# Kernel tuning notes

Measured on AMD Instinct MI355X. Metric: run time of the kernel, lower is better.

The kernel has to match this reference:

```python
import jax, jax.numpy as jnp
import numpy as np
import math

D_MODEL = 1024
NUM_HEADS = 16
D_K = D_MODEL // NUM_HEADS
THETA = 10000.0
B, T = 2, 2048


def _trunc_normal(key, shape, std):
    # truncated normal in [-3std, 3std]
    return jax.random.truncated_normal(key, -3.0, 3.0, shape, jnp.float32) * std


def setup_inputs() -> dict:
    key = jax.random.key(0)
    ks = jax.random.split(key, 6)
    sigma = math.sqrt(2.0 / (D_MODEL + D_MODEL))
    x = jax.random.normal(ks[0], (B, T, D_MODEL), jnp.float32)
    Wq = _trunc_normal(ks[1], (D_MODEL, D_MODEL), sigma)  # [out, in]
    Wk = _trunc_normal(ks[2], (D_MODEL, D_MODEL), sigma)
    Wv = _trunc_normal(ks[3], (D_MODEL, D_MODEL), sigma)
    Wo = _trunc_normal(ks[4], (D_MODEL, D_MODEL), sigma)
    token_positions = jnp.arange(T, dtype=jnp.int64 if jax.config.read('jax_enable_x64') else jnp.int32)
    return {"x": x, "Wq": Wq, "Wk": Wk, "Wv": Wv, "Wo": Wo,
            "token_positions": token_positions}


def _rotate_half(x):
    x0 = x[..., ::2]
    x1 = x[..., 1::2]
    return jnp.stack((-x1, x0), axis=-1).reshape(x.shape)


def _rope(x, token_positions):
    # x: [B, H, T, d_k]; token_positions: [T]
    inv_freq = 1.0 / (THETA ** (jnp.arange(0, D_K, 2, dtype=jnp.float32) / D_K))
    ang = token_positions.astype(jnp.float32)[:, None] * inv_freq  # [T, d_k/2]
    cos = jnp.repeat(jnp.cos(ang), 2, axis=-1)  # [T, d_k]
    sin = jnp.repeat(jnp.sin(ang), 2, axis=-1)
    xdtype = x.dtype
    xf = x.astype(jnp.float32)
    return (xf * cos + _rotate_half(xf) * sin).astype(xdtype)


def reference(x, Wq, Wk, Wv, Wo, token_positions):
    b, t, _ = x.shape

    def proj_split(W):
        h = jnp.einsum('btd,od->bto', x, W)
        return h.reshape(b, t, NUM_HEADS, D_K).transpose(0, 2, 1, 3)  # [B,H,T,d_k]

    Q = _rope(proj_split(Wq), token_positions)
    K = _rope(proj_split(Wk), token_positions)
    V = proj_split(Wv)

    scores = jnp.einsum('bhqd,bhkd->bhqk', Q, K) / math.sqrt(D_K)
    causal = jnp.tril(jnp.ones((t, t), dtype=bool))  # [T,T]
    scores = jnp.where(causal, scores, -jnp.inf)
    weights = jax.nn.softmax(scores, axis=-1)
    attn = jnp.einsum('bhqk,bhkd->bhqd', weights, V)  # [B,H,T,d_v]
    merged = attn.transpose(0, 2, 1, 3).reshape(b, t, D_MODEL)
    return jnp.einsum('btd,od->bto', merged, Wo)
```

## Files before the change

### kernel.cpp

```cpp
#include <hip/hip_runtime.h>
#include <hip/hip_fp16.h>
#include <cstdint>
#include <cstddef>

#define DMODEL 1024
#define NHEADS 16
#define DKH    64
#define SEQT   2048
#define NBATCH 2
#define MTOT   (NBATCH*SEQT)

#define QSCALE 0.1803368801111204f

using h16   = _Float16;
using h16x2 = __attribute__((ext_vector_type(2))) h16;
using h16x4 = __attribute__((ext_vector_type(4))) h16;
using h16x8 = __attribute__((ext_vector_type(8))) h16;
using f32x4 = __attribute__((ext_vector_type(4))) float;
using fp16x2_native = __attribute__((ext_vector_type(2))) __fp16;

using as1_void = __attribute__((address_space(1))) void;
using as3_void = __attribute__((address_space(3))) void;

__device__ __forceinline__ void gll16(void* lds, const void* g) {
  __builtin_amdgcn_global_load_lds((const as1_void*)g, (as3_void*)lds, 16, 0, 0);
}

__device__ __forceinline__ h16x2 pkrtz(float a, float b) {
  fp16x2_native t = __builtin_amdgcn_cvt_pkrtz(a, b);
  h16x2 r; r[0] = (h16)t[0]; r[1] = (h16)t[1]; return r;
}

__device__ __forceinline__ h16 hx2exp(h16 x) {
  __half r = hexp2(*(__half*)&x);
  return *(h16*)&r;
}

__device__ __forceinline__ h16x4 cvt4(const float4 v) {
  h16x4 o; o[0] = (h16)v.x; o[1] = (h16)v.y; o[2] = (h16)v.z; o[3] = (h16)v.w; return o;
}

__global__ void prep_kernel(const float4* __restrict__ x,
                            const float4* __restrict__ Wq, const float4* __restrict__ Wk,
                            const float4* __restrict__ Wv, const float4* __restrict__ Wo,
                            h16x4* __restrict__ xb,
                            h16x4* __restrict__ wqb, h16x4* __restrict__ wkb,
                            h16x4* __restrict__ wvb, h16x4* __restrict__ wob,
                            float* __restrict__ ctab, float* __restrict__ stab) {
  const int tid  = blockIdx.x * blockDim.x + threadIdx.x;
  const int nthr = gridDim.x * blockDim.x;
  const int NX4 = MTOT * DMODEL / 4;
  const int NW4 = DMODEL * DMODEL / 4;
  for (int i = tid; i < NX4; i += nthr) xb[i] = cvt4(x[i]);
  for (int i = tid; i < NW4; i += nthr) {
    wqb[i] = cvt4(Wq[i]);
    wkb[i] = cvt4(Wk[i]);
    wvb[i] = cvt4(Wv[i]);
    wob[i] = cvt4(Wo[i]);
  }
  for (int i = tid; i < SEQT * 32; i += nthr) {
    const int t = i >> 5, fi = i & 31;
    float inv = __expf(-0.28782313662425575f * (float)fi);
    float ang = (float)t * inv;
    float s, c;
    sincosf(ang, &s, &c);
    ctab[i] = c; stab[i] = s;
  }
}

__device__ __forceinline__ void gemm128_bt(const h16* __restrict__ A, const h16* __restrict__ Bt,
                                           int m0, int n0, h16* Al, h16* Bl, f32x4 acc[4][4]) {
  const int tid  = threadIdx.x;
  const int lane = tid & 63;
  const int wv   = tid >> 6;
  const int wm = (wv >> 1) * 64, wn = (wv & 1) * 64;
  const int lr = lane & 15, lk = (lane >> 4) * 8;
  const int srow = tid >> 2, scol = (tid & 3) * 8;
  const h16* a0 = A  + (size_t)(m0 + srow) * DMODEL + scol;
  const h16* a1 = a0 + (size_t)64 * DMODEL;
  const h16* b0 = Bt + (size_t)(n0 + srow) * DMODEL + scol;
  const h16* b1 = b0 + (size_t)64 * DMODEL;
  h16* alds0 = Al + wv * 512;
  h16* alds1 = Al + 2048 + wv * 512;
  h16* blds0 = Bl + wv * 512;
  h16* blds1 = Bl + 2048 + wv * 512;

  for (int k0 = 0; k0 < DMODEL; k0 += 32) {
    __syncthreads();
    gll16(alds0, a0 + k0);
    gll16(alds1, a1 + k0);
    gll16(blds0, b0 + k0);
    gll16(blds1, b1 + k0);
    __syncthreads();
    h16x8 af[4], bfr[4];
#pragma unroll
    for (int i = 0; i < 4; ++i) {
      af[i]  = *(const h16x8*)(Al + (wm + i * 16 + lr) * 32 + lk);
      bfr[i] = *(const h16x8*)(Bl + (wn + i * 16 + lr) * 32 + lk);
    }
#pragma unroll
    for (int i = 0; i < 4; ++i)
#pragma unroll
      for (int j = 0; j < 4; ++j)
        acc[i][j] = __builtin_amdgcn_mfma_f32_16x16x32_f16(af[i], bfr[j], acc[i][j], 0, 0, 0);
  }
}

__global__ __launch_bounds__(256, 2) void qkv_kernel(
    const h16* __restrict__ xb,
    const h16* __restrict__ wqb, const h16* __restrict__ wkb, const h16* __restrict__ wvb,
    const float* __restrict__ ctab, const float* __restrict__ stab,
    h16* __restrict__ Qb, h16* __restrict__ Kb, h16* __restrict__ Vt) {
  __shared__ h16 Al[128 * 32], Bl[128 * 32];
  const int which = blockIdx.z;
  const h16* W = (which == 0) ? wqb : (which == 1) ? wkb : wvb;
  const int m0 = blockIdx.x * 128, n0 = blockIdx.y * 128;
  f32x4 acc[4][4];
  const f32x4 zero4 = {0.f, 0.f, 0.f, 0.f};
#pragma unroll
  for (int i = 0; i < 4; ++i)
#pragma unroll
    for (int j = 0; j < 4; ++j) acc[i][j] = zero4;

  gemm128_bt(xb, W, m0, n0, Al, Bl, acc);

  const int lane = threadIdx.x & 63, wv = threadIdx.x >> 6;
  const int wm = (wv >> 1) * 64, wn = (wv & 1) * 64;
  const int lr4 = ((lane >> 4) << 2), lc = lane & 15;
  if (which == 2) {
#pragma unroll
    for (int i = 0; i < 4; ++i) {
      const int m = m0 + wm + i * 16 + lr4;
      const int b = m >> 11, t = m & (SEQT - 1);
#pragma unroll
      for (int j = 0; j < 4; ++j) {
        const int n = n0 + wn + j * 16 + lc;
        const int h = n >> 6, d = n & 63;
        h16x4 o4;
#pragma unroll
        for (int r = 0; r < 4; ++r) o4[r] = (h16)acc[i][j][r];
        *(h16x4*)&Vt[((size_t)(b * NHEADS + h) * DKH + d) * SEQT + t] = o4;
      }
    }
  } else {
#pragma unroll
    for (int i = 0; i < 4; ++i) {
#pragma unroll
      for (int j = 0; j < 4; ++j) {
        const int n = n0 + wn + j * 16 + lc;
        const int h = n >> 6, d = n & 63;
#pragma unroll
        for (int r = 0; r < 4; ++r) {
          const int m = m0 + wm + i * 16 + lr4 + r;
          const int b = m >> 11, t = m & (SEQT - 1);
          float v = acc[i][j][r];
          float pv = __shfl_xor(v, 1);
          const int fi = d >> 1;
          float c = ctab[t * 32 + fi], s = stab[t * 32 + fi];
          float res = (d & 1) ? (v * c + pv * s) : (v * c - pv * s);
          if (which == 0) res *= QSCALE;
          h16* dst = (which == 0) ? Qb : Kb;
          dst[((size_t)(b * NHEADS + h) * SEQT + t) * DKH + d] = (h16)res;
        }
      }
    }
  }
}

__global__ __launch_bounds__(256, 4) void attn_kernel(
    const h16* __restrict__ Qb, const h16* __restrict__ Kb,
    const h16* __restrict__ Vt, h16* __restrict__ Mg) {
  __shared__ h16 Kl[128][76];
  __shared__ h16 Vl[64][140];
  const int linear = blockIdx.x + 32 * blockIdx.y;
  const int v   = linear & 7;
  const int p   = linear >> 3;
  const int w   = p >> 5;
  const int c32 = p & 31;
  const int u   = (c32 + w) & 3;
  const int bh  = c32;
  const int qt  = (u == 0) ? v : (u == 1) ? (15 - v) : (u == 2) ? (16 + v) : (31 - v);
  const int b = bh >> 4, h = bh & 15;
  const int tid = threadIdx.x, lane = tid & 63, wv = tid >> 6;
  const int lr = lane & 15, lg = lane >> 4;
  const int q0 = qt * 64;
  const int qbase = q0 + wv * 16;
  const int q = qbase + lr;
  const h16* Qp = Qb + ((size_t)bh * SEQT + qbase) * DKH;
  const h16* Kp = Kb + (size_t)bh * SEQT * DKH;
  const h16* Vp = Vt + (size_t)bh * DKH * SEQT;

  h16x8 qf[2];
#pragma unroll
  for (int kk = 0; kk < 2; ++kk)
    qf[kk] = *(const h16x8*)(Qp + lr * DKH + kk * 32 + lg * 8);

  float mrow = -3.0e38f, lsum = 0.f;
  f32x4 o[4];
  const f32x4 zero4 = {0.f, 0.f, 0.f, 0.f};
#pragma unroll
  for (int di = 0; di < 4; ++di) o[di] = zero4;

  const int sr = tid >> 2, sc = (tid & 3) * 16;
  uint4 ka0, ka1, ka2, ka3;
  uint4 va0, va1, va2, va3;

#define KISSUE(k0_) {                                                      \
    const h16* kb_ = Kp + (size_t)(k0_) * DKH;                             \
    ka0 = *(const uint4*)(kb_ + (size_t)sr * DKH + sc);                    \
    ka1 = *(const uint4*)(kb_ + (size_t)sr * DKH + sc + 8);                \
    ka2 = *(const uint4*)(kb_ + (size_t)(64 + sr) * DKH + sc);             \
    ka3 = *(const uint4*)(kb_ + (size_t)(64 + sr) * DKH + sc + 8);         \
  }
#define KWRITE() {                                                         \
    *(uint4*)&Kl[sr][sc]          = ka0;                                   \
    *(uint4*)&Kl[sr][sc + 8]      = ka1;                                   \
    *(uint4*)&Kl[64 + sr][sc]     = ka2;                                   \
    *(uint4*)&Kl[64 + sr][sc + 8] = ka3;                                   \
  }
#define VISSUE(k0_) {                                                      \
    const h16* vb_ = Vp + (k0_);                                           \
    va0 = *(const uint4*)(vb_ + (size_t)sr * SEQT + sc);                   \
    va1 = *(const uint4*)(vb_ + (size_t)sr * SEQT + sc + 8);               \
    va2 = *(const uint4*)(vb_ + (size_t)sr * SEQT + 64 + sc);              \
    va3 = *(const uint4*)(vb_ + (size_t)sr * SEQT + 64 + sc + 8);          \
  }
#define VWRITE() {                                                         \
    *(uint4*)&Vl[sr][sc]          = va0;                                   \
    *(uint4*)&Vl[sr][sc + 8]      = va1;                                   \
    *(uint4*)&Vl[sr][64 + sc]     = va2;                                   \
    *(uint4*)&Vl[sr][64 + sc + 8] = va3;                                   \
  }

  KISSUE(0); VISSUE(0);
  KWRITE(); VWRITE();
  __syncthreads();

  const int nkt = (qt >> 1) + 1;
  for (int kt = 0; kt < nkt; ++kt) {
    const int k0 = kt * 128;
    const bool more = (kt + 1 < nkt);

    if (more) { KISSUE(k0 + 128); __builtin_amdgcn_sched_barrier(0); }

    f32x4 s[8];
    __builtin_amdgcn_s_setprio(1);
#pragma unroll
    for (int ni = 0; ni < 8; ++ni) {
      s[ni] = zero4;
#pragma unroll
      for (int kk = 0; kk < 2; ++kk) {
        h16x8 kf = *(const h16x8*)&Kl[ni * 16 + lr][kk * 32 + lg * 8];
        s[ni] = __builtin_amdgcn_mfma_f32_16x16x32_f16(kf, qf[kk], s[ni], 0, 0, 0);
      }
    }
    __builtin_amdgcn_s_setprio(0);

    __syncthreads();
    if (more) {
      KWRITE();
      VISSUE(k0 + 128); __builtin_amdgcn_sched_barrier(0);
    }

    if (kt == nkt - 1) {
#pragma unroll
      for (int ni = 0; ni < 8; ++ni)
#pragma unroll
        for (int r = 0; r < 4; ++r) {
          const int key = k0 + ni * 16 + lg * 4 + r;
          if (key > q) s[ni][r] = -3.0e38f;
        }
    }

    h16x4 s16[8];
#pragma unroll
    for (int ni = 0; ni < 8; ++ni) {
      h16x2 lo = pkrtz(s[ni][0], s[ni][1]);
      h16x2 hi = pkrtz(s[ni][2], s[ni][3]);
      s16[ni][0] = lo[0]; s16[ni][1] = lo[1]; s16[ni][2] = hi[0]; s16[ni][3] = hi[1];
    }

    h16x4 t0 = __builtin_elementwise_max(s16[0], s16[1]);
    h16x4 t1 = __builtin_elementwise_max(s16[2], s16[3]);
    h16x4 t2 = __builtin_elementwise_max(s16[4], s16[5]);
    h16x4 t3 = __builtin_elementwise_max(s16[6], s16[7]);
    h16x4 t4 = __builtin_elementwise_max(__builtin_elementwise_max(t0, t1),
                                         __builtin_elementwise_max(t2, t3));
    h16 mh = t4[0] > t4[1] ? t4[0] : t4[1];
    h16 m2 = t4[2] > t4[3] ? t4[2] : t4[3];
    mh = mh > m2 ? mh : m2;
    float mx = (float)mh;
    mx = fmaxf(mx, __shfl_xor(mx, 16));
    mx = fmaxf(mx, __shfl_xor(mx, 32));
    if (mx > mrow + 9.0f) {
      const float scl = exp2f(mrow - mx);
      mrow = mx;
      lsum *= scl;
#pragma unroll
      for (int di = 0; di < 4; ++di)
#pragma unroll
        for (int r = 0; r < 4; ++r) o[di][r] *= scl;
    }

    const h16 m16 = (h16)mrow;
    h16x4 mv; mv[0] = m16; mv[1] = m16; mv[2] = m16; mv[3] = m16;
    h16x4 pb[8];
#pragma unroll
    for (int ni = 0; ni < 8; ++ni) {
      h16x4 d = s16[ni] - mv;
      pb[ni][0] = hx2exp(d[0]); pb[ni][1] = hx2exp(d[1]);
      pb[ni][2] = hx2exp(d[2]); pb[ni][3] = hx2exp(d[3]);
    }

    {
      h16x4 a0 = pb[0] + pb[1];
      h16x4 a1 = pb[2] + pb[3];
      h16x4 a2 = pb[4] + pb[5];
      h16x4 a3 = pb[6] + pb[7];
      h16x4 a4 = (a0 + a1) + (a2 + a3);
      float rs = (float)a4[0] + (float)a4[1] + (float)a4[2] + (float)a4[3];
      rs += __shfl_xor(rs, 16);
      rs += __shfl_xor(rs, 32);
      lsum += rs;
    }

    __builtin_amdgcn_s_setprio(1);
#pragma unroll
    for (int ni = 0; ni < 8; ++ni) {
#pragma unroll
      for (int di = 0; di < 4; ++di) {
        h16x4 va = *(const h16x4*)&Vl[di * 16 + lr][ni * 16 + lg * 4];
        o[di] = __builtin_amdgcn_mfma_f32_16x16x16f16(va, pb[ni], o[di], 0, 0, 0);
      }
    }
    __builtin_amdgcn_s_setprio(0);

    __syncthreads();
    if (more) VWRITE();
  }
#undef KISSUE
#undef KWRITE
#undef VISSUE
#undef VWRITE

  __syncthreads();
  const float inv = 1.0f / lsum;
#pragma unroll
  for (int di = 0; di < 4; ++di) {
    h16x2 lo = pkrtz(o[di][0] * inv, o[di][1] * inv);
    h16x2 hi = pkrtz(o[di][2] * inv, o[di][3] * inv);
    h16x4 o4; o4[0] = lo[0]; o4[1] = lo[1]; o4[2] = hi[0]; o4[3] = hi[1];
    *(h16x4*)&Kl[wv * 16 + lr][di * 16 + lg * 4] = o4;
  }
  __syncthreads();
  {
    const int row = tid >> 2, c0 = (tid & 3) * 16;
    h16* dst = Mg + ((size_t)(b * SEQT + q0 + row)) * DMODEL + h * DKH + c0;
    *(uint4*)dst       = *(const uint4*)&Kl[row][c0];
    *(uint4*)(dst + 8) = *(const uint4*)&Kl[row][c0 + 8];
  }
}

__global__ __launch_bounds__(256, 2) void proj_kernel(
    const h16* __restrict__ Mg, const h16* __restrict__ wob, float* __restrict__ out) {
  __shared__ h16 Al[128 * 32], Bl[128 * 32];
  const int m0 = blockIdx.x * 128, n0 = blockIdx.y * 128;
  f32x4 acc[4][4];
  const f32x4 zero4 = {0.f, 0.f, 0.f, 0.f};
#pragma unroll
  for (int i = 0; i < 4; ++i)
#pragma unroll
    for (int j = 0; j < 4; ++j) acc[i][j] = zero4;

  gemm128_bt(Mg, wob, m0, n0, Al, Bl, acc);

  const int lane = threadIdx.x & 63, wv = threadIdx.x >> 6;
  const int wm = (wv >> 1) * 64, wn = (wv & 1) * 64;
  const int lr4 = ((lane >> 4) << 2), lc = lane & 15;
#pragma unroll
  for (int i = 0; i < 4; ++i)
#pragma unroll
    for (int j = 0; j < 4; ++j) {
      const int n = n0 + wn + j * 16 + lc;
#pragma unroll
      for (int r = 0; r < 4; ++r) {
        const int m = m0 + wm + i * 16 + lr4 + r;
        out[(size_t)m * DMODEL + n] = acc[i][j][r];
      }
    }
}

extern "C" void kernel_launch(void* const* d_in, const int* in_sizes, int n_in,
                              void* d_out, int out_size, void* d_ws, size_t ws_size,
                              hipStream_t stream) {
  (void)in_sizes; (void)n_in; (void)out_size; (void)ws_size;
  const float* x  = (const float*)d_in[0];
  const float* Wq = (const float*)d_in[1];
  const float* Wk = (const float*)d_in[2];
  const float* Wv = (const float*)d_in[3];
  const float* Wo = (const float*)d_in[4];
  float* out = (float*)d_out;

  char* w = (char*)d_ws;
  h16* xb  = (h16*)w; w += (size_t)MTOT * DMODEL * 2;
  h16* wqb = (h16*)w; w += (size_t)DMODEL * DMODEL * 2;
  h16* wkb = (h16*)w; w += (size_t)DMODEL * DMODEL * 2;
  h16* wvb = (h16*)w; w += (size_t)DMODEL * DMODEL * 2;
  h16* wob = (h16*)w; w += (size_t)DMODEL * DMODEL * 2;
  h16* Qb  = (h16*)w; w += (size_t)MTOT * DMODEL * 2;
  h16* Kb  = (h16*)w; w += (size_t)MTOT * DMODEL * 2;
  h16* Vt  = (h16*)w; w += (size_t)MTOT * DMODEL * 2;
  h16* Mg  = (h16*)w; w += (size_t)MTOT * DMODEL * 2;
  float* ctab = (float*)w; w += (size_t)SEQT * 32 * 4;
  float* stab = (float*)w; w += (size_t)SEQT * 32 * 4;

  prep_kernel<<<1024, 256, 0, stream>>>((const float4*)x, (const float4*)Wq, (const float4*)Wk,
                                        (const float4*)Wv, (const float4*)Wo,
                                        (h16x4*)xb, (h16x4*)wqb, (h16x4*)wkb, (h16x4*)wvb,
                                        (h16x4*)wob, ctab, stab);
  qkv_kernel<<<dim3(32, 8, 3), 256, 0, stream>>>(xb, wqb, wkb, wvb, ctab, stab, Qb, Kb, Vt);
  attn_kernel<<<dim3(32, 32), 256, 0, stream>>>(Qb, Kb, Vt, Mg);
  proj_kernel<<<dim3(32, 8), 256, 0, stream>>>(Mg, wob, out);
}
```

Measured before the change: 110.3 us.

## Split attention KV loop across warp pairs with split-K merge in LDS

The attention kernel now handles 32-query tiles and splits each tile's key/value range between two warp pairs. Each pair processes alternating 64-key tiles in its own LDS buffers. The partial softmax states (max, sum, output) are then merged through shared memory before the output is written. The grid doubles to 2048 blocks, aiming for more parallelism and better load balance across the causal triangle. The cost is extra LDS traffic for the merge, extra barriers, and idle iterations for one pair when the tile count is odd.

```diff
diff --git a/kernel.cpp b/kernel.cpp
--- a/kernel.cpp
+++ b/kernel.cpp
@@ -168,26 +168,26 @@
 }
 
 __global__ __launch_bounds__(256, 4) void attn_kernel(
-    const h16* __restrict__ Qb, const h16* __restrict__ Kb,
+    const h16* __restrict__ Qb, const h16* __restrict__ Kg,
     const h16* __restrict__ Vt, h16* __restrict__ Mg) {
-  __shared__ h16 Kl[128][76];
-  __shared__ h16 Vl[64][140];
-  const int linear = blockIdx.x + 32 * blockIdx.y;
-  const int v   = linear & 7;
-  const int p   = linear >> 3;
-  const int w   = p >> 5;
-  const int c32 = p & 31;
-  const int u   = (c32 + w) & 3;
-  const int bh  = c32;
-  const int qt  = (u == 0) ? v : (u == 1) ? (15 - v) : (u == 2) ? (16 + v) : (31 - v);
+  __shared__ h16 KT[2][64][76];
+  __shared__ h16 VT[2][64][76];
+  const int linear = blockIdx.x + 64 * blockIdx.y;
+  const int v  = linear & 7;
+  const int pp = linear >> 3;
+  const int bh = pp & 31;
+  const int j  = ((pp >> 5) + bh) & 7;
+  const int a  = (j & 1) ? ((j >> 1) * 16 + 15 - v) : ((j >> 1) * 16 + v);
   const int b = bh >> 4, h = bh & 15;
   const int tid = threadIdx.x, lane = tid & 63, wv = tid >> 6;
+  const int pair = wv & 1, sub = wv >> 1;
   const int lr = lane & 15, lg = lane >> 4;
-  const int q0 = qt * 64;
-  const int qbase = q0 + wv * 16;
-  const int q = qbase + lr;
-  const h16* Qp = Qb + ((size_t)bh * SEQT + qbase) * DKH;
-  const h16* Kp = Kb + (size_t)bh * SEQT * DKH;
+  const int q0 = a * 32;
+  const int q  = q0 + sub * 16 + lr;
+  const int nkt = (a >> 1) + 1;
+  const int T   = (nkt + 1) >> 1;
+  const h16* Qp = Qb + ((size_t)bh * SEQT + q0 + sub * 16) * DKH;
+  const h16* Kp = Kg + (size_t)bh * SEQT * DKH;
   const h16* Vp = Vt + (size_t)bh * DKH * SEQT;
 
   h16x8 qf[2];
@@ -201,142 +201,140 @@
 #pragma unroll
   for (int di = 0; di < 4; ++di) o[di] = zero4;
 
-  const int sr = tid >> 2, sc = (tid & 3) * 16;
+  const int tid2 = (sub << 6) | lane;
+  const int srow = tid2 >> 1, scol = (tid2 & 1) * 32;
   uint4 ka0, ka1, ka2, ka3;
   uint4 va0, va1, va2, va3;
 
 #define KISSUE(k0_) {                                                      \
-    const h16* kb_ = Kp + (size_t)(k0_) * DKH;                             \
-    ka0 = *(const uint4*)(kb_ + (size_t)sr * DKH + sc);                    \
-    ka1 = *(const uint4*)(kb_ + (size_t)sr * DKH + sc + 8);                \
-    ka2 = *(const uint4*)(kb_ + (size_t)(64 + sr) * DKH + sc);             \
-    ka3 = *(const uint4*)(kb_ + (size_t)(64 + sr) * DKH + sc + 8);         \
+    const h16* kb_ = Kp + (size_t)((k0_) + srow) * DKH + scol;             \
+    ka0 = *(const uint4*)(kb_);                                            \
+    ka1 = *(const uint4*)(kb_ + 8);                                        \
+    ka2 = *(const uint4*)(kb_ + 16);                                       \
+    ka3 = *(const uint4*)(kb_ + 24);                                       \
   }
 #define KWRITE() {                                                         \
-    *(uint4*)&Kl[sr][sc]          = ka0;                                   \
-    *(uint4*)&Kl[sr][sc + 8]      = ka1;                                   \
-    *(uint4*)&Kl[64 + sr][sc]     = ka2;                                   \
-    *(uint4*)&Kl[64 + sr][sc + 8] = ka3;                                   \
+    *(uint4*)&KT[pair][srow][scol]      = ka0;                             \
+    *(uint4*)&KT[pair][srow][scol + 8]  = ka1;                             \
+    *(uint4*)&KT[pair][srow][scol + 16] = ka2;                             \
+    *(uint4*)&KT[pair][srow][scol + 24] = ka3;                             \
   }
 #define VISSUE(k0_) {                                                      \
-    const h16* vb_ = Vp + (k0_);                                           \
-    va0 = *(const uint4*)(vb_ + (size_t)sr * SEQT + sc);                   \
-    va1 = *(const uint4*)(vb_ + (size_t)sr * SEQT + sc + 8);               \
-    va2 = *(const uint4*)(vb_ + (size_t)sr * SEQT + 64 + sc);              \
-    va3 = *(const uint4*)(vb_ + (size_t)sr * SEQT + 64 + sc + 8);          \
+    const h16* vb_ = Vp + (size_t)srow * SEQT + (k0_) + scol;              \
+    va0 = *(const uint4*)(vb_);                                            \
+    va1 = *(const uint4*)(vb_ + 8);                                        \
+    va2 = *(const uint4*)(vb_ + 16);                                       \
+    va3 = *(const uint4*)(vb_ + 24);                                       \
   }
 #define VWRITE() {                                                         \
-    *(uint4*)&Vl[sr][sc]          = va0;                                   \
-    *(uint4*)&Vl[sr][sc + 8]      = va1;                                   \
-    *(uint4*)&Vl[sr][64 + sc]     = va2;                                   \
-    *(uint4*)&Vl[sr][64 + sc + 8] = va3;                                   \
-  }
-
-  KISSUE(0); VISSUE(0);
-  KWRITE(); VWRITE();
+    *(uint4*)&VT[pair][srow][scol]      = va0;                             \
+    *(uint4*)&VT[pair][srow][scol + 8]  = va1;                             \
+    *(uint4*)&VT[pair][srow][scol + 16] = va2;                             \
+    *(uint4*)&VT[pair][srow][scol + 24] = va3;                             \
+  }
+
+  int kt = pair;
+  if (kt < nkt) {
+    KISSUE(kt * 64); VISSUE(kt * 64);
+    KWRITE(); VWRITE();
+  }
   __syncthreads();
 
-  const int nkt = (qt >> 1) + 1;
-  for (int kt = 0; kt < nkt; ++kt) {
-    const int k0 = kt * 128;
-    const bool more = (kt + 1 < nkt);
-
-    if (more) { KISSUE(k0 + 128); __builtin_amdgcn_sched_barrier(0); }
-
-    f32x4 s[8];
-    __builtin_amdgcn_s_setprio(1);
-#pragma unroll
-    for (int ni = 0; ni < 8; ++ni) {
-      s[ni] = zero4;
-#pragma unroll
-      for (int kk = 0; kk < 2; ++kk) {
-        h16x8 kf = *(const h16x8*)&Kl[ni * 16 + lr][kk * 32 + lg * 8];
-        s[ni] = __builtin_amdgcn_mfma_f32_16x16x32_f16(kf, qf[kk], s[ni], 0, 0, 0);
-      }
-    }
-    __builtin_amdgcn_s_setprio(0);
+  for (int t = 0; t < T; ++t, kt += 2) {
+    const bool active = (kt < nkt);
+    const bool hn = (kt + 2 < nkt);
+    const int k0 = kt * 64;
+
+    if (hn) { KISSUE((kt + 2) * 64); __builtin_amdgcn_sched_barrier(0); }
+
+    f32x4 s[4];
+    if (active) {
+      __builtin_amdgcn_s_setprio(1);
+#pragma unroll
+      for (int ni = 0; ni < 4; ++ni) {
+        s[ni] = zero4;
+#pragma unroll
+        for (int kk = 0; kk < 2; ++kk) {
+          h16x8 kf = *(const h16x8*)&KT[pair][ni * 16 + lr][kk * 32 + lg * 8];
+          s[ni] = __builtin_amdgcn_mfma_f32_16x16x32_f16(kf, qf[kk], s[ni], 0, 0, 0);
+        }
+      }
+      __builtin_amdgcn_s_setprio(0);
+    }
 
     __syncthreads();
-    if (more) {
+    if (hn) {
       KWRITE();
-      VISSUE(k0 + 128); __builtin_amdgcn_sched_barrier(0);
-    }
-
-    if (kt == nkt - 1) {
-#pragma unroll
-      for (int ni = 0; ni < 8; ++ni)
-#pragma unroll
-        for (int r = 0; r < 4; ++r) {
-          const int key = k0 + ni * 16 + lg * 4 + r;
-          if (key > q) s[ni][r] = -3.0e38f;
+      VISSUE((kt + 2) * 64); __builtin_amdgcn_sched_barrier(0);
+    }
+
+    if (active) {
+      if (kt == nkt - 1) {
+#pragma unroll
+        for (int ni = 0; ni < 4; ++ni)
+#pragma unroll
+          for (int r = 0; r < 4; ++r) {
+            const int key = k0 + ni * 16 + lg * 4 + r;
+            if (key > q) s[ni][r] = -3.0e38f;
+          }
+      }
+
+      h16x4 s16[4];
+#pragma unroll
+      for (int ni = 0; ni < 4; ++ni) {
+        h16x2 lo = pkrtz(s[ni][0], s[ni][1]);
+        h16x2 hi = pkrtz(s[ni][2], s[ni][3]);
+        s16[ni][0] = lo[0]; s16[ni][1] = lo[1]; s16[ni][2] = hi[0]; s16[ni][3] = hi[1];
+      }
+      h16x4 t0 = __builtin_elementwise_max(s16[0], s16[1]);
+      h16x4 t1 = __builtin_elementwise_max(s16[2], s16[3]);
+      h16x4 t4 = __builtin_elementwise_max(t0, t1);
+      h16 mh = t4[0] > t4[1] ? t4[0] : t4[1];
+      h16 m2 = t4[2] > t4[3] ? t4[2] : t4[3];
+      mh = mh > m2 ? mh : m2;
+      float mx = (float)mh;
+      mx = fmaxf(mx, __shfl_xor(mx, 16));
+      mx = fmaxf(mx, __shfl_xor(mx, 32));
+      if (mx > mrow + 9.0f) {
+        const float scl = exp2f(mrow - mx);
+        mrow = mx;
+        lsum *= scl;
+#pragma unroll
+        for (int di = 0; di < 4; ++di)
+#pragma unroll
+          for (int r = 0; r < 4; ++r) o[di][r] *= scl;
+      }
+      const h16 m16 = (h16)mrow;
+      h16x4 mv; mv[0] = m16; mv[1] = m16; mv[2] = m16; mv[3] = m16;
+      h16x4 pb[4];
+#pragma unroll
+      for (int ni = 0; ni < 4; ++ni) {
+        h16x4 d = s16[ni] - mv;
+        pb[ni][0] = hx2exp(d[0]); pb[ni][1] = hx2exp(d[1]);
+        pb[ni][2] = hx2exp(d[2]); pb[ni][3] = hx2exp(d[3]);
+      }
+      {
+        h16x4 a4 = (pb[0] + pb[1]) + (pb[2] + pb[3]);
+        float rs = (float)a4[0] + (float)a4[1] + (float)a4[2] + (float)a4[3];
+        rs += __shfl_xor(rs, 16);
+        rs += __shfl_xor(rs, 32);
+        lsum += rs;
+      }
+
+      __builtin_amdgcn_s_setprio(1);
+#pragma unroll
+      for (int ni = 0; ni < 4; ++ni) {
+#pragma unroll
+        for (int di = 0; di < 4; ++di) {
+          h16x4 va = *(const h16x4*)&VT[pair][di * 16 + lr][ni * 16 + lg * 4];
+          o[di] = __builtin_amdgcn_mfma_f32_16x16x16f16(va, pb[ni], o[di], 0, 0, 0);
         }
-    }
-
-    h16x4 s16[8];
-#pragma unroll
-    for (int ni = 0; ni < 8; ++ni) {
-      h16x2 lo = pkrtz(s[ni][0], s[ni][1]);
-      h16x2 hi = pkrtz(s[ni][2], s[ni][3]);
-      s16[ni][0] = lo[0]; s16[ni][1] = lo[1]; s16[ni][2] = hi[0]; s16[ni][3] = hi[1];
-    }
-
-    h16x4 t0 = __builtin_elementwise_max(s16[0], s16[1]);
-    h16x4 t1 = __builtin_elementwise_max(s16[2], s16[3]);
-    h16x4 t2 = __builtin_elementwise_max(s16[4], s16[5]);
-    h16x4 t3 = __builtin_elementwise_max(s16[6], s16[7]);
-    h16x4 t4 = __builtin_elementwise_max(__builtin_elementwise_max(t0, t1),
-                                         __builtin_elementwise_max(t2, t3));
-    h16 mh = t4[0] > t4[1] ? t4[0] : t4[1];
-    h16 m2 = t4[2] > t4[3] ? t4[2] : t4[3];
-    mh = mh > m2 ? mh : m2;
-    float mx = (float)mh;
-    mx = fmaxf(mx, __shfl_xor(mx, 16));
-    mx = fmaxf(mx, __shfl_xor(mx, 32));
-    if (mx > mrow + 9.0f) {
-      const float scl = exp2f(mrow - mx);
-      mrow = mx;
-      lsum *= scl;
-#pragma unroll
-      for (int di = 0; di < 4; ++di)
-#pragma unroll
-        for (int r = 0; r < 4; ++r) o[di][r] *= scl;
-    }
-
-    const h16 m16 = (h16)mrow;
-    h16x4 mv; mv[0] = m16; mv[1] = m16; mv[2] = m16; mv[3] = m16;
-    h16x4 pb[8];
-#pragma unroll
-    for (int ni = 0; ni < 8; ++ni) {
-      h16x4 d = s16[ni] - mv;
-      pb[ni][0] = hx2exp(d[0]); pb[ni][1] = hx2exp(d[1]);
-      pb[ni][2] = hx2exp(d[2]); pb[ni][3] = hx2exp(d[3]);
-    }
-
-    {
-      h16x4 a0 = pb[0] + pb[1];
-      h16x4 a1 = pb[2] + pb[3];
-      h16x4 a2 = pb[4] + pb[5];
-      h16x4 a3 = pb[6] + pb[7];
-      h16x4 a4 = (a0 + a1) + (a2 + a3);
-      float rs = (float)a4[0] + (float)a4[1] + (float)a4[2] + (float)a4[3];
-      rs += __shfl_xor(rs, 16);
-      rs += __shfl_xor(rs, 32);
-      lsum += rs;
-    }
-
-    __builtin_amdgcn_s_setprio(1);
-#pragma unroll
-    for (int ni = 0; ni < 8; ++ni) {
-#pragma unroll
-      for (int di = 0; di < 4; ++di) {
-        h16x4 va = *(const h16x4*)&Vl[di * 16 + lr][ni * 16 + lg * 4];
-        o[di] = __builtin_amdgcn_mfma_f32_16x16x16f16(va, pb[ni], o[di], 0, 0, 0);
-      }
-    }
-    __builtin_amdgcn_s_setprio(0);
+      }
+      __builtin_amdgcn_s_setprio(0);
+    }
 
     __syncthreads();
-    if (more) VWRITE();
+    if (hn) VWRITE();
   }
 #undef KISSUE
 #undef KWRITE
@@ -344,20 +342,42 @@
 #undef VWRITE
 
   __syncthreads();
-  const float inv = 1.0f / lsum;
-#pragma unroll
-  for (int di = 0; di < 4; ++di) {
-    h16x2 lo = pkrtz(o[di][0] * inv, o[di][1] * inv);
-    h16x2 hi = pkrtz(o[di][2] * inv, o[di][3] * inv);
-    h16x4 o4; o4[0] = lo[0]; o4[1] = lo[1]; o4[2] = hi[0]; o4[3] = hi[1];
-    *(h16x4*)&Kl[wv * 16 + lr][di * 16 + lg * 4] = o4;
+  float* mf = (float*)&KT[0][0][0];
+  float* mm = mf + 2048;
+  float* ml = mm + 32;
+  const int row = sub * 16 + lr;
+  if (pair == 1) {
+#pragma unroll
+    for (int di = 0; di < 4; ++di)
+#pragma unroll
+      for (int r = 0; r < 4; ++r)
+        mf[row * 64 + di * 16 + lg * 4 + r] = o[di][r];
+    if (lg == 0) { mm[row] = mrow; ml[row] = lsum; }
+  }
+  __syncthreads();
+  h16* ob = &VT[0][0][0];
+  if (pair == 0) {
+    const float m1 = mm[row], l1 = ml[row];
+    const float mM = fmaxf(mrow, m1);
+    const float c0 = exp2f(mrow - mM), c1 = exp2f(m1 - mM);
+    const float inv = 1.0f / (lsum * c0 + l1 * c1);
+#pragma unroll
+    for (int di = 0; di < 4; ++di) {
+      float r0 = (o[di][0] * c0 + mf[row * 64 + di * 16 + lg * 4 + 0] * c1) * inv;
+      float r1 = (o[di][1] * c0 + mf[row * 64 + di * 16 + lg * 4 + 1] * c1) * inv;
+      float r2 = (o[di][2] * c0 + mf[row * 64 + di * 16 + lg * 4 + 2] * c1) * inv;
+      float r3 = (o[di][3] * c0 + mf[row * 64 + di * 16 + lg * 4 + 3] * c1) * inv;
+      h16x2 lo = pkrtz(r0, r1);
+      h16x2 hi = pkrtz(r2, r3);
+      h16x4 o4; o4[0] = lo[0]; o4[1] = lo[1]; o4[2] = hi[0]; o4[3] = hi[1];
+      *(h16x4*)&ob[row * 76 + di * 16 + lg * 4] = o4;
+    }
   }
   __syncthreads();
   {
-    const int row = tid >> 2, c0 = (tid & 3) * 16;
-    h16* dst = Mg + ((size_t)(b * SEQT + q0 + row)) * DMODEL + h * DKH + c0;
-    *(uint4*)dst       = *(const uint4*)&Kl[row][c0];
-    *(uint4*)(dst + 8) = *(const uint4*)&Kl[row][c0 + 8];
+    const int orow = tid >> 3, c0b = (tid & 7) * 8;
+    h16* dst = Mg + ((size_t)(b * SEQT + q0 + orow)) * DMODEL + h * DKH + c0b;
+    *(uint4*)dst = *(const uint4*)&ob[orow * 76 + c0b];
   }
 }
 
@@ -419,6 +439,6 @@
                                         (h16x4*)xb, (h16x4*)wqb, (h16x4*)wkb, (h16x4*)wvb,
                                         (h16x4*)wob, ctab, stab);
   qkv_kernel<<<dim3(32, 8, 3), 256, 0, stream>>>(xb, wqb, wkb, wvb, ctab, stab, Qb, Kb, Vt);
-  attn_kernel<<<dim3(32, 32), 256, 0, stream>>>(Qb, Kb, Vt, Mg);
+  attn_kernel<<<dim3(64, 32), 256, 0, stream>>>(Qb, Kb, Vt, Mg);
   proj_kernel<<<dim3(32, 8), 256, 0, stream>>>(Mg, wob, out);
 }
```

Measured after the change: 142.9 us. 29.6% more time.
